# Kernel optimization log

Hardware: AMD Instinct MI355X
Metric: run time of the kernel (lower is better)

## Reference

```python
import jax, jax.numpy as jnp
import numpy as np

N_HEAD = 16
N_EMBD = 1024
BLOCK = 2048
B, T = 4, 2048


def setup_inputs() -> dict:
    key = jax.random.key(0)
    ks = jax.random.split(key, 5)
    s = 0.02
    return {
        "x": jax.random.normal(ks[0], (B, T, N_EMBD), dtype=jnp.float32),
        "qkv_w": jax.random.normal(ks[1], (3 * N_EMBD, N_EMBD), dtype=jnp.float32) * s,
        "qkv_b": jnp.zeros((3 * N_EMBD,), dtype=jnp.float32),
        "proj_w": jax.random.normal(ks[2], (N_EMBD, N_EMBD), dtype=jnp.float32) * s,
        "proj_b": jnp.zeros((N_EMBD,), dtype=jnp.float32),
    }


def reference(x, qkv_w, qkv_b, proj_w, proj_b):
    Bx, Tx, C = x.shape
    hd = C // N_HEAD
    qkv = x @ qkv_w.T + qkv_b  # [B,T,3C]
    q, k, v = jnp.split(qkv, 3, axis=-1)
    # [B,T,C] -> [B,H,T,hd]
    def heads(t):
        return t.reshape(Bx, Tx, N_HEAD, hd).transpose(0, 2, 1, 3)
    q, k, v = heads(q), heads(k), heads(v)
    scores = jnp.einsum("bhqd,bhkd->bhqk", q, k) / jnp.sqrt(jnp.float32(hd))
    causal = jnp.tril(jnp.ones((Tx, Tx), dtype=bool))
    scores = jnp.where(causal[None, None, :, :], scores, -jnp.inf)
    attn = jax.nn.softmax(scores, axis=-1)
    out = jnp.einsum("bhqk,bhkd->bhqd", attn, v)
    out = out.transpose(0, 2, 1, 3).reshape(Bx, Tx, C)
    return out @ proj_w.T + proj_b
```

## Files before the change

### kernel.cpp

```cpp
#include <hip/hip_runtime.h>
#include <stdint.h>
#include <math.h>

#define DEVI __device__ __forceinline__

typedef __attribute__((ext_vector_type(8))) short bf16x8;
typedef __attribute__((ext_vector_type(4))) float f32x4;

DEVI unsigned short f2bf(float f) {
  union { float f; unsigned u; } v; v.f = f;
  unsigned u = v.u;
  u += 0x7fffu + ((u >> 16) & 1u);
  return (unsigned short)(u >> 16);
}

DEVI unsigned cvt_pk_bf16(float a, float b) {
  unsigned r;
  asm("v_cvt_pk_bf16_f32 %0, %1, %2" : "=v"(r) : "v"(a), "v"(b));
  return r;
}

DEVI f32x4 mfma16(bf16x8 a, bf16x8 b, f32x4 c) {
  return __builtin_amdgcn_mfma_f32_16x16x32_bf16(a, b, c, 0, 0, 0);
}

DEVI void gld16(const unsigned short* g, unsigned short* l) {
  __builtin_amdgcn_global_load_lds(
      (const __attribute__((address_space(1))) unsigned int*)(uintptr_t)g,
      (__attribute__((address_space(3))) unsigned int*)(unsigned int)(uintptr_t)l,
      16, 0, 0);
}

#define VMCNT(n) asm volatile("s_waitcnt vmcnt(" #n ")" ::: "memory")
#define BAR()                              \
  do {                                     \
    __builtin_amdgcn_s_barrier();          \
    __builtin_amdgcn_sched_barrier(0);     \
  } while (0)

__global__ __launch_bounds__(256) void cvt3_kernel(
    const float* __restrict__ a, unsigned short* __restrict__ oa,
    const float* __restrict__ b, unsigned short* __restrict__ ob,
    const float* __restrict__ c, unsigned short* __restrict__ oc) {
  int bid = blockIdx.x;
  const float* in; unsigned short* out; int i;
  if (bid < 8192)       { in = a; out = oa; i = bid; }
  else if (bid < 11264) { in = b; out = ob; i = bid - 8192; }
  else                  { in = c; out = oc; i = bid - 11264; }
  int idx = (i * 256 + (int)threadIdx.x) * 4;
  float4 v = *(const float4*)(in + idx);
  unsigned lo = f2bf(v.x) | ((unsigned)f2bf(v.y) << 16);
  unsigned hi = f2bf(v.z) | ((unsigned)f2bf(v.w) << 16);
  uint2 o; o.x = lo; o.y = hi;
  *(uint2*)(out + idx) = o;
}

template <int MODE>
__global__ __launch_bounds__(512, 2) void gemm8(
    const unsigned short* __restrict__ A, const unsigned short* __restrict__ Bw,
    const float* __restrict__ bias, float* __restrict__ Cf,
    unsigned short* __restrict__ Qo, unsigned short* __restrict__ Ko,
    unsigned short* __restrict__ Vo, int M, int N, int K, int nbx) {
  extern __shared__ unsigned short lds[];
  const int tid = threadIdx.x;
  const int lane = tid & 63;
  const int w = tid >> 6;
  const int wm = w >> 2, wn = w & 3;
  const int lr = lane & 15, lq = lane >> 4;

  const int cpx = gridDim.x >> 3;
  const int swz = (blockIdx.x & 7) * cpx + (blockIdx.x >> 3);
  const int bx = swz % nbx, by = swz / nbx;
  const int m0 = by * 256, n0 = bx * 256;

  const int sr = lane >> 3;
  const int sc = ((lane & 7) ^ sr) << 3;
  const unsigned short* pa = A + (size_t)(m0 + sr) * K + sc;
  const unsigned short* pb = Bw + (size_t)(n0 + sr) * K + sc;

  const int aA0 = w, aA1 = 16 + w;
  const int aB0 = 8 + w, aB1 = 24 + w;
  const int bA0 = (w & 3) + ((w >> 2) << 3), bA1 = bA0 + 16;
  const int bB0 = bA0 + 4, bB1 = bA1 + 4;

  const int bs0 = (lq ^ (lr & 7)) << 3;
  const int bs1 = ((lq + 4) ^ (lr & 7)) << 3;

  f32x4 acc[8][4] = {};

  auto sA = [&](int buf, int kt, int c) {
    gld16(pa + (size_t)(c << 3) * K + kt, lds + buf * 32768 + (c << 9));
  };
  auto sB = [&](int buf, int kt, int c) {
    gld16(pb + (size_t)(c << 3) * K + kt, lds + buf * 32768 + 16384 + (c << 9));
  };

#define LDA(A_, mh)                                                          \
  _Pragma("unroll") for (int i = 0; i < 4; ++i) {                            \
    int ar = wm * 128 + (mh) * 64 + i * 16 + lr;                             \
    A_[i][0] = *(const bf16x8*)(As_ + ar * 64 + bs0);                        \
    A_[i][1] = *(const bf16x8*)(As_ + ar * 64 + bs1);                        \
  }
#define LDB(B_, nh)                                                          \
  _Pragma("unroll") for (int j = 0; j < 2; ++j) {                            \
    int br = wn * 64 + (nh) * 32 + j * 16 + lr;                              \
    B_[j][0] = *(const bf16x8*)(Bs_ + br * 64 + bs0);                        \
    B_[j][1] = *(const bf16x8*)(Bs_ + br * 64 + bs1);                        \
  }
#define MM(A_, B_, mh, nh)                                                   \
  __builtin_amdgcn_s_setprio(1);                                             \
  _Pragma("unroll") for (int i = 0; i < 4; ++i)                              \
    _Pragma("unroll") for (int j = 0; j < 2; ++j) {                          \
      acc[(mh) * 4 + i][(nh) * 2 + j] =                                      \
          mfma16(A_[i][0], B_[j][0], acc[(mh) * 4 + i][(nh) * 2 + j]);       \
      acc[(mh) * 4 + i][(nh) * 2 + j] =                                      \
          mfma16(A_[i][1], B_[j][1], acc[(mh) * 4 + i][(nh) * 2 + j]);       \
    }                                                                        \
  __builtin_amdgcn_s_setprio(0);

  sA(0, 0, aA0); sA(0, 0, aA1);
  sB(0, 0, bA0); sB(0, 0, bA1);
  sB(0, 0, bB0); sB(0, 0, bB1);
  sA(0, 0, aB0); sA(0, 0, aB1);
  VMCNT(4);
  BAR();

  const int NT = K >> 6;
  for (int t = 0; t < NT - 1; ++t) {
    const int buf = t & 1, nb = buf ^ 1;
    const int kt = (t + 1) << 6;
    const unsigned short* As_ = lds + buf * 32768;
    const unsigned short* Bs_ = As_ + 16384;
    bf16x8 af[4][2], b0f[2][2], b1f[2][2];
    sA(nb, kt, aA0); sA(nb, kt, aA1);
    LDA(af, 0); LDB(b0f, 0);
    MM(af, b0f, 0, 0);
    VMCNT(4); BAR();
    sB(nb, kt, bA0); sB(nb, kt, bA1);
    LDB(b1f, 1);
    MM(af, b1f, 0, 1);
    VMCNT(4); BAR();
    sB(nb, kt, bB0); sB(nb, kt, bB1);
    LDA(af, 1);
    MM(af, b1f, 1, 1);
    sA(nb, kt, aB0); sA(nb, kt, aB1);
    MM(af, b0f, 1, 0);
    VMCNT(4); BAR();
  }
  {
    const int buf = (NT - 1) & 1;
    const unsigned short* As_ = lds + buf * 32768;
    const unsigned short* Bs_ = As_ + 16384;
    bf16x8 af[4][2], b0f[2][2], b1f[2][2];
    LDA(af, 0); LDB(b0f, 0);
    MM(af, b0f, 0, 0);
    VMCNT(2); BAR();
    LDB(b1f, 1);
    MM(af, b1f, 0, 1);
    VMCNT(0); BAR();
    LDA(af, 1);
    MM(af, b1f, 1, 1);
    MM(af, b0f, 1, 0);
  }
#undef LDA
#undef LDB
#undef MM

#pragma unroll
  for (int mt = 0; mt < 8; ++mt) {
#pragma unroll
    for (int nt = 0; nt < 4; ++nt) {
      int n_g = n0 + wn * 64 + nt * 16 + lr;
      float bv = bias[n_g];
      if (MODE == 1) {
#pragma unroll
        for (int r = 0; r < 4; ++r) {
          int m_g = m0 + wm * 128 + mt * 16 + lq * 4 + r;
          Cf[(size_t)m_g * N + n_g] = acc[mt][nt][r] + bv;
        }
      } else {
        int which = n_g >> 10;
        int rem = n_g & 1023;
        int h = rem >> 6, d = rem & 63;
        int m_base = m0 + wm * 128 + mt * 16 + lq * 4;
        int b = m_base >> 11, tt = m_base & 2047;
        if (which == 2) {
          uint2 pv;
          pv.x = cvt_pk_bf16(acc[mt][nt][0] + bv, acc[mt][nt][1] + bv);
          pv.y = cvt_pk_bf16(acc[mt][nt][2] + bv, acc[mt][nt][3] + bv);
          *(uint2*)(Vo + (((size_t)(b * 16 + h) * 64 + d) * 2048 + tt)) = pv;
        } else {
          unsigned short* p = (which == 0) ? Qo : Ko;
#pragma unroll
          for (int r = 0; r < 4; ++r) {
            size_t idx = (((size_t)(b * 16 + h) * 2048) + tt + r) * 64 + d;
            p[idx] = f2bf(acc[mt][nt][r] + bv);
          }
        }
      }
    }
  }
}

__global__ __launch_bounds__(512, 2) void attn_kernel(
    const unsigned short* __restrict__ Q, const unsigned short* __restrict__ K,
    const unsigned short* __restrict__ V, unsigned short* __restrict__ Y) {
  constexpr int T = 2048, HD = 64, H = 16;
  __shared__ unsigned short Kt[2][64 * 72];
  __shared__ unsigned short Vt[2][64 * 72];
  __shared__ unsigned short Pt[8][16 * 72];

  const int tid = threadIdx.x;
  const int lane = tid & 63;
  const int w = tid >> 6;
  const int lr = lane & 15, lq = lane >> 4;
  const int pair = blockIdx.x;
  const int h = blockIdx.y;
  const int b = blockIdx.z;
  const size_t bh = (size_t)(b * H + h) * T * HD;
  const float SC = 0.125f * 1.44269504089f;

  const int krow = tid >> 3, kcb = (tid & 7) << 3;

  float4 kr, vr;
  auto load_tile = [&](int jt) {
    const int c0 = jt * 64;
    kr = *(const float4*)(K + bh + (size_t)(c0 + krow) * HD + kcb);
    vr = *(const float4*)(V + bh + (size_t)krow * T + c0 + kcb);
  };
  auto stage = [&](int buf) {
    *(float4*)(&Kt[buf][krow * 72 + kcb]) = kr;
    *(float4*)(&Vt[buf][krow * 72 + kcb]) = vr;
  };

  load_tile(0);

  for (int phase = 0; phase < 2; ++phase) {
    const int qt = phase ? (7 - pair) : pair;
    const int q0 = qt * 256;
    const int nkv = 4 * (qt + 1);
    const int qw = q0 + w * 32;

    bf16x8 qf[2][2];
#pragma unroll
    for (int qs = 0; qs < 2; ++qs)
#pragma unroll
      for (int kb = 0; kb < 2; ++kb)
        qf[qs][kb] = *(const bf16x8*)(Q + bh + (size_t)(qw + qs * 16 + lr) * HD +
                                      kb * 32 + lq * 8);

    f32x4 o[2][4] = {};
    float mi[2] = {-INFINITY, -INFINITY}, li[2] = {0.f, 0.f};

    stage(0);
    load_tile(1);
    __syncthreads();

    for (int jt = 0; jt < nkv; ++jt) {
      const int c0 = jt * 64;
      const int buf = jt & 1;

      if (c0 <= qw + 31) {
        f32x4 s[2][4];
        __builtin_amdgcn_s_setprio(1);
#pragma unroll
        for (int nt = 0; nt < 4; ++nt) {
          bf16x8 kf0 = *(const bf16x8*)(&Kt[buf][(nt * 16 + lr) * 72 + lq * 8]);
          bf16x8 kf1 = *(const bf16x8*)(&Kt[buf][(nt * 16 + lr) * 72 + 32 + lq * 8]);
#pragma unroll
          for (int qs = 0; qs < 2; ++qs) {
            f32x4 z = {};
            z = mfma16(kf0, qf[qs][0], z);
            s[qs][nt] = mfma16(kf1, qf[qs][1], z);
          }
        }
        __builtin_amdgcn_s_setprio(0);
        if (c0 + 63 > qw) {
#pragma unroll
          for (int qs = 0; qs < 2; ++qs) {
            int qg = qw + qs * 16 + lr;
#pragma unroll
            for (int nt = 0; nt < 4; ++nt)
#pragma unroll
              for (int r = 0; r < 4; ++r) {
                int kvg = c0 + nt * 16 + lq * 4 + r;
                if (kvg > qg) s[qs][nt][r] = -INFINITY;
              }
          }
        }
        float mxs[2];
#pragma unroll
        for (int qs = 0; qs < 2; ++qs) {
          float mx = -INFINITY;
#pragma unroll
          for (int nt = 0; nt < 4; ++nt)
            mx = fmaxf(mx, fmaxf(fmaxf(s[qs][nt][0], s[qs][nt][1]),
                                 fmaxf(s[qs][nt][2], s[qs][nt][3])));
          mx = fmaxf(mx, __shfl_xor(mx, 16));
          mx = fmaxf(mx, __shfl_xor(mx, 32));
          mxs[qs] = mx * SC;
        }
        if (!__all((mxs[0] <= mi[0] + 8.f) && (mxs[1] <= mi[1] + 8.f))) {
#pragma unroll
          for (int qs = 0; qs < 2; ++qs) {
            float mnew = fmaxf(mi[qs], mxs[qs]);
            float alpha = __builtin_amdgcn_exp2f(mi[qs] - mnew);
            mi[qs] = mnew;
            li[qs] *= alpha;
#pragma unroll
            for (int nt = 0; nt < 4; ++nt)
#pragma unroll
              for (int r = 0; r < 4; ++r) o[qs][nt][r] *= alpha;
          }
        }
        bf16x8 pf[2][2];
#pragma unroll
        for (int qs = 0; qs < 2; ++qs) {
          float rs = 0.f;
#pragma unroll
          for (int nt = 0; nt < 4; ++nt) {
            float p0 = __builtin_amdgcn_exp2f(fmaf(s[qs][nt][0], SC, -mi[qs]));
            float p1 = __builtin_amdgcn_exp2f(fmaf(s[qs][nt][1], SC, -mi[qs]));
            float p2 = __builtin_amdgcn_exp2f(fmaf(s[qs][nt][2], SC, -mi[qs]));
            float p3 = __builtin_amdgcn_exp2f(fmaf(s[qs][nt][3], SC, -mi[qs]));
            rs += (p0 + p1) + (p2 + p3);
            uint2 pk;
            pk.x = cvt_pk_bf16(p0, p1);
            pk.y = cvt_pk_bf16(p2, p3);
            *(uint2*)(&Pt[w][lr * 72 + nt * 16 + lq * 4]) = pk;
          }
          li[qs] += rs;
#pragma unroll
          for (int kb = 0; kb < 2; ++kb)
            pf[qs][kb] = *(const bf16x8*)(&Pt[w][lr * 72 + kb * 32 + lq * 8]);
        }
        __builtin_amdgcn_s_setprio(1);
#pragma unroll
        for (int nt = 0; nt < 4; ++nt) {
          bf16x8 vf0 = *(const bf16x8*)(&Vt[buf][(nt * 16 + lr) * 72 + lq * 8]);
          bf16x8 vf1 = *(const bf16x8*)(&Vt[buf][(nt * 16 + lr) * 72 + 32 + lq * 8]);
#pragma unroll
          for (int qs = 0; qs < 2; ++qs) {
            o[qs][nt] = mfma16(vf0, pf[qs][0], o[qs][nt]);
            o[qs][nt] = mfma16(vf1, pf[qs][1], o[qs][nt]);
          }
        }
        __builtin_amdgcn_s_setprio(0);
      }

      if (jt + 1 < nkv) {
        stage(buf ^ 1);
        if (jt + 2 < nkv) load_tile(jt + 2);
        else if (phase == 0) load_tile(0);
        __syncthreads();
      }
    }

#pragma unroll
    for (int qs = 0; qs < 2; ++qs) {
      float l = li[qs];
      l += __shfl_xor(l, 16);
      l += __shfl_xor(l, 32);
      float inv = 1.f / l;
      int t_g = qw + qs * 16 + lr;
#pragma unroll
      for (int nt = 0; nt < 4; ++nt) {
        uint2 yv;
        yv.x = cvt_pk_bf16(o[qs][nt][0] * inv, o[qs][nt][1] * inv);
        yv.y = cvt_pk_bf16(o[qs][nt][2] * inv, o[qs][nt][3] * inv);
        *(uint2*)(Y + ((size_t)(b * T + t_g)) * 1024 + h * 64 + nt * 16 + lq * 4) = yv;
      }
    }
  }
}

extern "C" void kernel_launch(void* const* d_in, const int* in_sizes, int n_in,
                              void* d_out, int out_size, void* d_ws, size_t ws_size,
                              hipStream_t stream) {
  const float* x = (const float*)d_in[0];
  const float* qkv_w = (const float*)d_in[1];
  const float* qkv_b = (const float*)d_in[2];
  const float* proj_w = (const float*)d_in[3];
  const float* proj_b = (const float*)d_in[4];
  float* out = (float*)d_out;

  unsigned short* ws = (unsigned short*)d_ws;
  unsigned short* xb = ws;
  unsigned short* wqkv = xb + 8388608;
  unsigned short* wproj = wqkv + 3145728;
  unsigned short* Qb = wproj + 1048576;
  unsigned short* Kb = Qb + 8388608;
  unsigned short* Vb = Kb + 8388608;
  unsigned short* Yb = Vb + 8388608;

  auto* g0 = gemm8<0>;
  auto* g1 = gemm8<1>;
  static bool attr_set = false;
  if (!attr_set) {
    (void)hipFuncSetAttribute((const void*)g0,
                              hipFuncAttributeMaxDynamicSharedMemorySize, 131072);
    (void)hipFuncSetAttribute((const void*)g1,
                              hipFuncAttributeMaxDynamicSharedMemorySize, 131072);
    attr_set = true;
  }

  cvt3_kernel<<<12288, 256, 0, stream>>>(x, xb, qkv_w, wqkv, proj_w, wproj);

  gemm8<0><<<dim3(384), 512, 131072, stream>>>(xb, wqkv, qkv_b, nullptr, Qb, Kb, Vb,
                                               8192, 3072, 1024, 12);
  attn_kernel<<<dim3(4, 16, 4), 512, 0, stream>>>(Qb, Kb, Vb, Yb);
  gemm8<1><<<dim3(128), 512, 131072, stream>>>(Yb, wproj, proj_b, out, nullptr, nullptr,
                                               nullptr, 8192, 1024, 1024, 4);
}
```

Before: 246.5 us.

## Switch GEMMs to 4-stage K=32 pipeline and halve proj GEMM N tile

Replaces the double-buffered K=64 staging with a four-buffer, K=32 pipeline that keeps three tiles of loads in flight and needs one barrier per step instead of three. The XOR swizzle on LDS is dropped. The projection GEMM now uses 256x128 tiles, so it launches 256 blocks instead of 128 and fills more CUs on a small problem. The cost is smaller K steps with a higher ratio of loads to MFMAs, possible LDS bank conflicts from the unswizzled layout, and more A-tile reloads in the projection.

```diff
diff --git a/kernel.cpp b/kernel.cpp
--- a/kernel.cpp
+++ b/kernel.cpp
@@ -55,13 +55,14 @@
   *(uint2*)(out + idx) = o;
 }
 
-template <int MODE>
+template <int MODE, int NBH>
 __global__ __launch_bounds__(512, 2) void gemm8(
     const unsigned short* __restrict__ A, const unsigned short* __restrict__ Bw,
     const float* __restrict__ bias, float* __restrict__ Cf,
     unsigned short* __restrict__ Qo, unsigned short* __restrict__ Ko,
     unsigned short* __restrict__ Vo, int M, int N, int K, int nbx) {
   extern __shared__ unsigned short lds[];
+  constexpr int BUFS = 8192 + 4096 * NBH;
   const int tid = threadIdx.x;
   const int lane = tid & 63;
   const int w = tid >> 6;
@@ -71,96 +72,76 @@
   const int cpx = gridDim.x >> 3;
   const int swz = (blockIdx.x & 7) * cpx + (blockIdx.x >> 3);
   const int bx = swz % nbx, by = swz / nbx;
-  const int m0 = by * 256, n0 = bx * 256;
-
-  const int sr = lane >> 3;
-  const int sc = ((lane & 7) ^ sr) << 3;
-  const unsigned short* pa = A + (size_t)(m0 + sr) * K + sc;
-  const unsigned short* pb = Bw + (size_t)(n0 + sr) * K + sc;
-
-  const int aA0 = w, aA1 = 16 + w;
-  const int aB0 = 8 + w, aB1 = 24 + w;
-  const int bA0 = (w & 3) + ((w >> 2) << 3), bA1 = bA0 + 16;
-  const int bB0 = bA0 + 4, bB1 = bA1 + 4;
-
-  const int bs0 = (lq ^ (lr & 7)) << 3;
-  const int bs1 = ((lq + 4) ^ (lr & 7)) << 3;
-
-  f32x4 acc[8][4] = {};
+  const int m0 = by * 256, n0 = bx * (NBH * 128);
+
+  const unsigned short* pa = A + (size_t)(m0 + (lane >> 2)) * K + ((lane & 3) << 3);
+  const unsigned short* pb = Bw + (size_t)(n0 + (lane >> 2)) * K + ((lane & 3) << 3);
+
+  f32x4 acc[8][2 * NBH] = {};
 
   auto sA = [&](int buf, int kt, int c) {
-    gld16(pa + (size_t)(c << 3) * K + kt, lds + buf * 32768 + (c << 9));
+    gld16(pa + (size_t)(c << 4) * K + kt, lds + buf * BUFS + (c << 9));
   };
   auto sB = [&](int buf, int kt, int c) {
-    gld16(pb + (size_t)(c << 3) * K + kt, lds + buf * 32768 + 16384 + (c << 9));
+    gld16(pb + (size_t)(c << 4) * K + kt, lds + buf * BUFS + 8192 + (c << 9));
+  };
+  auto stage = [&](int buf, int t) {
+    const int kt = t << 5;
+    sA(buf, kt, w); sA(buf, kt, 8 + w);
+    sB(buf, kt, w);
+    if constexpr (NBH == 2) sB(buf, kt, 8 + w);
   };
 
 #define LDA(A_, mh)                                                          \
-  _Pragma("unroll") for (int i = 0; i < 4; ++i) {                            \
-    int ar = wm * 128 + (mh) * 64 + i * 16 + lr;                             \
-    A_[i][0] = *(const bf16x8*)(As_ + ar * 64 + bs0);                        \
-    A_[i][1] = *(const bf16x8*)(As_ + ar * 64 + bs1);                        \
-  }
+  _Pragma("unroll") for (int i = 0; i < 4; ++i)                              \
+    A_[i] = *(const bf16x8*)(As_ + (wm * 128 + (mh) * 64 + i * 16 + lr) * 32 \
+                             + lq * 8);
 #define LDB(B_, nh)                                                          \
-  _Pragma("unroll") for (int j = 0; j < 2; ++j) {                            \
-    int br = wn * 64 + (nh) * 32 + j * 16 + lr;                              \
-    B_[j][0] = *(const bf16x8*)(Bs_ + br * 64 + bs0);                        \
-    B_[j][1] = *(const bf16x8*)(Bs_ + br * 64 + bs1);                        \
-  }
+  _Pragma("unroll") for (int j = 0; j < 2; ++j)                              \
+    B_[j] = *(const bf16x8*)(Bs_ + (wn * (NBH * 32) + (nh) * 32 + j * 16     \
+                             + lr) * 32 + lq * 8);
 #define MM(A_, B_, mh, nh)                                                   \
   __builtin_amdgcn_s_setprio(1);                                             \
   _Pragma("unroll") for (int i = 0; i < 4; ++i)                              \
-    _Pragma("unroll") for (int j = 0; j < 2; ++j) {                          \
+    _Pragma("unroll") for (int j = 0; j < 2; ++j)                            \
       acc[(mh) * 4 + i][(nh) * 2 + j] =                                      \
-          mfma16(A_[i][0], B_[j][0], acc[(mh) * 4 + i][(nh) * 2 + j]);       \
-      acc[(mh) * 4 + i][(nh) * 2 + j] =                                      \
-          mfma16(A_[i][1], B_[j][1], acc[(mh) * 4 + i][(nh) * 2 + j]);       \
-    }                                                                        \
+          mfma16(A_[i], B_[j], acc[(mh) * 4 + i][(nh) * 2 + j]);             \
   __builtin_amdgcn_s_setprio(0);
 
-  sA(0, 0, aA0); sA(0, 0, aA1);
-  sB(0, 0, bA0); sB(0, 0, bA1);
-  sB(0, 0, bB0); sB(0, 0, bB1);
-  sA(0, 0, aB0); sA(0, 0, aB1);
-  VMCNT(4);
+  const int NT = K >> 5;
+  stage(0, 0); stage(1, 1); stage(2, 2);
+  if constexpr (NBH == 2) { VMCNT(8); } else { VMCNT(6); }
   BAR();
 
-  const int NT = K >> 6;
-  for (int t = 0; t < NT - 1; ++t) {
-    const int buf = t & 1, nb = buf ^ 1;
-    const int kt = (t + 1) << 6;
-    const unsigned short* As_ = lds + buf * 32768;
-    const unsigned short* Bs_ = As_ + 16384;
-    bf16x8 af[4][2], b0f[2][2], b1f[2][2];
-    sA(nb, kt, aA0); sA(nb, kt, aA1);
-    LDA(af, 0); LDB(b0f, 0);
-    MM(af, b0f, 0, 0);
-    VMCNT(4); BAR();
-    sB(nb, kt, bA0); sB(nb, kt, bA1);
-    LDB(b1f, 1);
-    MM(af, b1f, 0, 1);
-    VMCNT(4); BAR();
-    sB(nb, kt, bB0); sB(nb, kt, bB1);
-    LDA(af, 1);
-    MM(af, b1f, 1, 1);
-    sA(nb, kt, aB0); sA(nb, kt, aB1);
-    MM(af, b0f, 1, 0);
-    VMCNT(4); BAR();
-  }
-  {
-    const int buf = (NT - 1) & 1;
-    const unsigned short* As_ = lds + buf * 32768;
-    const unsigned short* Bs_ = As_ + 16384;
-    bf16x8 af[4][2], b0f[2][2], b1f[2][2];
-    LDA(af, 0); LDB(b0f, 0);
-    MM(af, b0f, 0, 0);
-    VMCNT(2); BAR();
-    LDB(b1f, 1);
-    MM(af, b1f, 0, 1);
-    VMCNT(0); BAR();
-    LDA(af, 1);
-    MM(af, b1f, 1, 1);
-    MM(af, b0f, 1, 0);
+  for (int t = 0; t < NT; ++t) {
+    if (t + 3 < NT) stage((t + 3) & 3, t + 3);
+    const unsigned short* As_ = lds + (t & 3) * BUFS;
+    const unsigned short* Bs_ = As_ + 8192;
+    bf16x8 af0[4], af1[4], b0[2];
+    if constexpr (NBH == 2) {
+      bf16x8 b1[2];
+      LDA(af0, 0); LDB(b0, 0);
+      MM(af0, b0, 0, 0);
+      LDB(b1, 1);
+      MM(af0, b1, 0, 1);
+      LDA(af1, 1);
+      MM(af1, b1, 1, 1);
+      MM(af1, b0, 1, 0);
+    } else {
+      LDA(af0, 0); LDB(b0, 0);
+      MM(af0, b0, 0, 0);
+      LDA(af1, 1);
+      MM(af1, b0, 1, 0);
+    }
+    if (t < NT - 3) {
+      if constexpr (NBH == 2) { VMCNT(8); } else { VMCNT(6); }
+      BAR();
+    } else if (t == NT - 3) {
+      if constexpr (NBH == 2) { VMCNT(4); } else { VMCNT(3); }
+      BAR();
+    } else if (t == NT - 2) {
+      VMCNT(0); BAR();
+    }
   }
 #undef LDA
 #undef LDB
@@ -169,8 +150,8 @@
 #pragma unroll
   for (int mt = 0; mt < 8; ++mt) {
 #pragma unroll
-    for (int nt = 0; nt < 4; ++nt) {
-      int n_g = n0 + wn * 64 + nt * 16 + lr;
+    for (int nt = 0; nt < 2 * NBH; ++nt) {
+      int n_g = n0 + wn * (NBH * 32) + nt * 16 + lr;
       float bv = bias[n_g];
       if (MODE == 1) {
 #pragma unroll
@@ -393,22 +374,22 @@
   unsigned short* Vb = Kb + 8388608;
   unsigned short* Yb = Vb + 8388608;
 
-  auto* g0 = gemm8<0>;
-  auto* g1 = gemm8<1>;
+  auto* g0 = gemm8<0, 2>;
+  auto* g1 = gemm8<1, 1>;
   static bool attr_set = false;
   if (!attr_set) {
     (void)hipFuncSetAttribute((const void*)g0,
                               hipFuncAttributeMaxDynamicSharedMemorySize, 131072);
     (void)hipFuncSetAttribute((const void*)g1,
-                              hipFuncAttributeMaxDynamicSharedMemorySize, 131072);
+                              hipFuncAttributeMaxDynamicSharedMemorySize, 98304);
     attr_set = true;
   }
 
   cvt3_kernel<<<12288, 256, 0, stream>>>(x, xb, qkv_w, wqkv, proj_w, wproj);
 
-  gemm8<0><<<dim3(384), 512, 131072, stream>>>(xb, wqkv, qkv_b, nullptr, Qb, Kb, Vb,
-                                               8192, 3072, 1024, 12);
+  gemm8<0, 2><<<dim3(384), 512, 131072, stream>>>(xb, wqkv, qkv_b, nullptr, Qb, Kb,
+                                                  Vb, 8192, 3072, 1024, 12);
   attn_kernel<<<dim3(4, 16, 4), 512, 0, stream>>>(Qb, Kb, Vb, Yb);
-  gemm8<1><<<dim3(128), 512, 131072, stream>>>(Yb, wproj, proj_b, out, nullptr, nullptr,
-                                               nullptr, 8192, 1024, 1024, 4);
-}
+  gemm8<1, 1><<<dim3(256), 512, 98304, stream>>>(Yb, wproj, proj_b, out, nullptr,
+                                                 nullptr, nullptr, 8192, 1024, 1024, 8);
+}
```

After: 256.0 us. +3.9%, slower.

## Shrink GEMM tile to 128x256 and use triple-buffered LDS pipeline

Applied to the files above, without the earlier changes.

The GEMM block tile is halved in M (256x256 to 128x256), doubling the grid to 768 and 256 blocks so more CUs are busy. The staging changes from an interleaved double buffer to a three-stage LDS ring that prefetches two k-tiles ahead with one barrier per iteration. This is meant to improve occupancy, wave coverage and latency hiding. In exchange, each block does less compute per loaded B tile, and dynamic LDS rises to 144KB, which may allow only one block per CU.

```diff
diff --git a/kernel.cpp b/kernel.cpp
--- a/kernel.cpp
+++ b/kernel.cpp
@@ -62,6 +62,7 @@
     unsigned short* __restrict__ Qo, unsigned short* __restrict__ Ko,
     unsigned short* __restrict__ Vo, int M, int N, int K, int nbx) {
   extern __shared__ unsigned short lds[];
+  constexpr int BUFS = 8192 + 16384;
   const int tid = threadIdx.x;
   const int lane = tid & 63;
   const int w = tid >> 6;
@@ -71,33 +72,33 @@
   const int cpx = gridDim.x >> 3;
   const int swz = (blockIdx.x & 7) * cpx + (blockIdx.x >> 3);
   const int bx = swz % nbx, by = swz / nbx;
-  const int m0 = by * 256, n0 = bx * 256;
+  const int m0 = by * 128, n0 = bx * 256;
 
   const int sr = lane >> 3;
   const int sc = ((lane & 7) ^ sr) << 3;
   const unsigned short* pa = A + (size_t)(m0 + sr) * K + sc;
   const unsigned short* pb = Bw + (size_t)(n0 + sr) * K + sc;
 
-  const int aA0 = w, aA1 = 16 + w;
-  const int aB0 = 8 + w, aB1 = 24 + w;
-  const int bA0 = (w & 3) + ((w >> 2) << 3), bA1 = bA0 + 16;
-  const int bB0 = bA0 + 4, bB1 = bA1 + 4;
-
   const int bs0 = (lq ^ (lr & 7)) << 3;
   const int bs1 = ((lq + 4) ^ (lr & 7)) << 3;
 
-  f32x4 acc[8][4] = {};
+  f32x4 acc[4][4] = {};
 
   auto sA = [&](int buf, int kt, int c) {
-    gld16(pa + (size_t)(c << 3) * K + kt, lds + buf * 32768 + (c << 9));
+    gld16(pa + (size_t)(c << 3) * K + kt, lds + buf * BUFS + (c << 9));
   };
   auto sB = [&](int buf, int kt, int c) {
-    gld16(pb + (size_t)(c << 3) * K + kt, lds + buf * 32768 + 16384 + (c << 9));
+    gld16(pb + (size_t)(c << 3) * K + kt, lds + buf * BUFS + 8192 + (c << 9));
+  };
+  auto stage = [&](int buf, int t) {
+    const int kt = t << 6;
+    sA(buf, kt, w); sA(buf, kt, 8 + w);
+    sB(buf, kt, w); sB(buf, kt, 8 + w); sB(buf, kt, 16 + w); sB(buf, kt, 24 + w);
   };
 
 #define LDA(A_, mh)                                                          \
-  _Pragma("unroll") for (int i = 0; i < 4; ++i) {                            \
-    int ar = wm * 128 + (mh) * 64 + i * 16 + lr;                             \
+  _Pragma("unroll") for (int i = 0; i < 2; ++i) {                            \
+    int ar = wm * 64 + (mh) * 32 + i * 16 + lr;                              \
     A_[i][0] = *(const bf16x8*)(As_ + ar * 64 + bs0);                        \
     A_[i][1] = *(const bf16x8*)(As_ + ar * 64 + bs1);                        \
   }
@@ -109,65 +110,47 @@
   }
 #define MM(A_, B_, mh, nh)                                                   \
   __builtin_amdgcn_s_setprio(1);                                             \
-  _Pragma("unroll") for (int i = 0; i < 4; ++i)                              \
+  _Pragma("unroll") for (int i = 0; i < 2; ++i)                              \
     _Pragma("unroll") for (int j = 0; j < 2; ++j) {                          \
-      acc[(mh) * 4 + i][(nh) * 2 + j] =                                      \
-          mfma16(A_[i][0], B_[j][0], acc[(mh) * 4 + i][(nh) * 2 + j]);       \
-      acc[(mh) * 4 + i][(nh) * 2 + j] =                                      \
-          mfma16(A_[i][1], B_[j][1], acc[(mh) * 4 + i][(nh) * 2 + j]);       \
+      acc[(mh) * 2 + i][(nh) * 2 + j] =                                      \
+          mfma16(A_[i][0], B_[j][0], acc[(mh) * 2 + i][(nh) * 2 + j]);       \
+      acc[(mh) * 2 + i][(nh) * 2 + j] =                                      \
+          mfma16(A_[i][1], B_[j][1], acc[(mh) * 2 + i][(nh) * 2 + j]);       \
     }                                                                        \
   __builtin_amdgcn_s_setprio(0);
 
-  sA(0, 0, aA0); sA(0, 0, aA1);
-  sB(0, 0, bA0); sB(0, 0, bA1);
-  sB(0, 0, bB0); sB(0, 0, bB1);
-  sA(0, 0, aB0); sA(0, 0, aB1);
-  VMCNT(4);
+  const int NT = K >> 6;
+  stage(0, 0); stage(1, 1);
+  VMCNT(6);
   BAR();
 
-  const int NT = K >> 6;
-  for (int t = 0; t < NT - 1; ++t) {
-    const int buf = t & 1, nb = buf ^ 1;
-    const int kt = (t + 1) << 6;
-    const unsigned short* As_ = lds + buf * 32768;
-    const unsigned short* Bs_ = As_ + 16384;
-    bf16x8 af[4][2], b0f[2][2], b1f[2][2];
-    sA(nb, kt, aA0); sA(nb, kt, aA1);
-    LDA(af, 0); LDB(b0f, 0);
-    MM(af, b0f, 0, 0);
-    VMCNT(4); BAR();
-    sB(nb, kt, bA0); sB(nb, kt, bA1);
-    LDB(b1f, 1);
-    MM(af, b1f, 0, 1);
-    VMCNT(4); BAR();
-    sB(nb, kt, bB0); sB(nb, kt, bB1);
-    LDA(af, 1);
-    MM(af, b1f, 1, 1);
-    sA(nb, kt, aB0); sA(nb, kt, aB1);
-    MM(af, b0f, 1, 0);
-    VMCNT(4); BAR();
-  }
-  {
-    const int buf = (NT - 1) & 1;
-    const unsigned short* As_ = lds + buf * 32768;
-    const unsigned short* Bs_ = As_ + 16384;
-    bf16x8 af[4][2], b0f[2][2], b1f[2][2];
-    LDA(af, 0); LDB(b0f, 0);
-    MM(af, b0f, 0, 0);
-    VMCNT(2); BAR();
-    LDB(b1f, 1);
-    MM(af, b1f, 0, 1);
-    VMCNT(0); BAR();
-    LDA(af, 1);
-    MM(af, b1f, 1, 1);
-    MM(af, b0f, 1, 0);
+  int cur = 0, sb = 2;
+  for (int t = 0; t < NT; ++t) {
+    if (t + 2 < NT) stage(sb, t + 2);
+    const unsigned short* As_ = lds + cur * BUFS;
+    const unsigned short* Bs_ = As_ + 8192;
+    bf16x8 a0[2][2], a1[2][2], b0[2][2], b1[2][2];
+    LDA(a0, 0); LDB(b0, 0);
+    MM(a0, b0, 0, 0);
+    LDB(b1, 1);
+    MM(a0, b1, 0, 1);
+    LDA(a1, 1);
+    MM(a1, b1, 1, 1);
+    MM(a1, b0, 1, 0);
+    if (t + 1 < NT) {
+      if (t + 2 < NT) { VMCNT(6); }
+      else            { VMCNT(0); }
+      BAR();
+    }
+    cur = (cur == 2) ? 0 : cur + 1;
+    sb = (sb == 2) ? 0 : sb + 1;
   }
 #undef LDA
 #undef LDB
 #undef MM
 
 #pragma unroll
-  for (int mt = 0; mt < 8; ++mt) {
+  for (int mt = 0; mt < 4; ++mt) {
 #pragma unroll
     for (int nt = 0; nt < 4; ++nt) {
       int n_g = n0 + wn * 64 + nt * 16 + lr;
@@ -175,14 +158,14 @@
       if (MODE == 1) {
 #pragma unroll
         for (int r = 0; r < 4; ++r) {
-          int m_g = m0 + wm * 128 + mt * 16 + lq * 4 + r;
+          int m_g = m0 + wm * 64 + mt * 16 + lq * 4 + r;
           Cf[(size_t)m_g * N + n_g] = acc[mt][nt][r] + bv;
         }
       } else {
         int which = n_g >> 10;
         int rem = n_g & 1023;
         int h = rem >> 6, d = rem & 63;
-        int m_base = m0 + wm * 128 + mt * 16 + lq * 4;
+        int m_base = m0 + wm * 64 + mt * 16 + lq * 4;
         int b = m_base >> 11, tt = m_base & 2047;
         if (which == 2) {
           uint2 pv;
@@ -398,17 +381,17 @@
   static bool attr_set = false;
   if (!attr_set) {
     (void)hipFuncSetAttribute((const void*)g0,
-                              hipFuncAttributeMaxDynamicSharedMemorySize, 131072);
+                              hipFuncAttributeMaxDynamicSharedMemorySize, 147456);
     (void)hipFuncSetAttribute((const void*)g1,
-                              hipFuncAttributeMaxDynamicSharedMemorySize, 131072);
+                              hipFuncAttributeMaxDynamicSharedMemorySize, 147456);
     attr_set = true;
   }
 
   cvt3_kernel<<<12288, 256, 0, stream>>>(x, xb, qkv_w, wqkv, proj_w, wproj);
 
-  gemm8<0><<<dim3(384), 512, 131072, stream>>>(xb, wqkv, qkv_b, nullptr, Qb, Kb, Vb,
-                                               8192, 3072, 1024, 12);
+  gemm8<0><<<dim3(768), 512, 147456, stream>>>(xb, wqkv, qkv_b, nullptr, Qb, Kb,
+                                               Vb, 8192, 3072, 1024, 12);
   attn_kernel<<<dim3(4, 16, 4), 512, 0, stream>>>(Qb, Kb, Vb, Yb);
-  gemm8<1><<<dim3(128), 512, 131072, stream>>>(Yb, wproj, proj_b, out, nullptr, nullptr,
-                                               nullptr, 8192, 1024, 1024, 4);
-}
+  gemm8<1><<<dim3(256), 512, 147456, stream>>>(Yb, wproj, proj_b, out, nullptr,
+                                               nullptr, nullptr, 8192, 1024, 1024, 4);
+}
```

New measurement: 262.7 us. +6.6%, slower.
